# Kernel optimization log

Hardware: AMD Instinct MI355X
Metric: run time of the kernel (lower is better)

The kernel has to match this reference:

```python
import jax, jax.numpy as jnp
import numpy as np

EMBED = 128
HIDDEN = 256
N_NODES = 50000
N_EDGES = 640000
LN_EPS = 1e-5


def setup_inputs() -> dict:
    key = jax.random.key(0)
    ks = jax.random.split(key, 10)
    node_embeddings = jax.random.normal(ks[0], (N_NODES, EMBED), dtype=jnp.float32)
    edge_embeddings = jax.random.normal(ks[1], (N_EDGES, EMBED), dtype=jnp.float32)
    edge_index_list = jax.random.randint(ks[2], (2, N_EDGES), 0, N_NODES, dtype=jnp.int64 if jax.config.jax_enable_x64 else jnp.int32)
    # LayerNorm params
    ln_gamma = jnp.ones((EMBED,), dtype=jnp.float32)
    ln_beta = jnp.zeros((EMBED,), dtype=jnp.float32)
    # phi: Linear(embed->hidden), Linear(hidden->embed); xavier-ish init
    W1 = jax.random.normal(ks[3], (EMBED, HIDDEN), dtype=jnp.float32) * (1.0 / np.sqrt(EMBED))
    b1 = jnp.zeros((HIDDEN,), dtype=jnp.float32)
    W2 = jax.random.normal(ks[4], (HIDDEN, EMBED), dtype=jnp.float32) * (1.0 / np.sqrt(HIDDEN))
    b2 = jnp.zeros((EMBED,), dtype=jnp.float32)
    # theta: Linear(embed->embed)
    Wt = jax.random.normal(ks[5], (EMBED, EMBED), dtype=jnp.float32) * (1.0 / np.sqrt(EMBED))
    bt = jnp.zeros((EMBED,), dtype=jnp.float32)
    return {
        "node_embeddings": node_embeddings,
        "edge_embeddings": edge_embeddings,
        "edge_index_list": edge_index_list,
        "ln_gamma": ln_gamma, "ln_beta": ln_beta,
        "W1": W1, "b1": b1, "W2": W2, "b2": b2,
        "Wt": Wt, "bt": bt,
    }


def _layer_norm(x, gamma, beta):
    mu = jnp.mean(x, axis=-1, keepdims=True)
    var = jnp.var(x, axis=-1, keepdims=True)
    return (x - mu) * jax.lax.rsqrt(var + LN_EPS) * gamma + beta


def reference(node_embeddings, edge_embeddings, edge_index_list,
              ln_gamma, ln_beta, W1, b1, W2, b2, Wt, bt):
    n_nodes = node_embeddings.shape[0]
    h = _layer_norm(node_embeddings, ln_gamma, ln_beta)  # [N, D]
    center = edge_index_list[0]    # [E]
    neighbor = edge_index_list[1]  # [E]
    h_c = h[center]                # [E, D] gather
    h_n = h[neighbor]              # [E, D] gather
    s = edge_embeddings + h_c + h_n  # [E, D]
    # phi: SiLU -> Linear -> SiLU -> Linear
    t = jax.nn.silu(s) @ W1 + b1          # [E, H]
    theta_edge = jax.nn.silu(t) @ W2 + b2  # [E, D]
    msg = h_n * theta_edge                 # [E, D]
    agg = jax.ops.segment_sum(msg, center, num_segments=n_nodes)  # [N, D]
    # theta: SiLU -> Linear
    out = jax.nn.silu(h + agg) @ Wt + bt   # [N, D]
    return out
```

## Files before the change

### kernel.cpp

```cpp
#include <hip/hip_runtime.h>
#include <hip/hip_bf16.h>
#include <stdint.h>

#define EMBED 128
#define HIDDEN 256

typedef __bf16 v8bf __attribute__((ext_vector_type(8)));
typedef float v4f __attribute__((ext_vector_type(4)));

__device__ __forceinline__ float bf2f(unsigned short u){
    union { uint32_t i; float f; } v; v.i = ((uint32_t)u) << 16; return v.f;
}
__device__ __forceinline__ unsigned short f2bf(float f){
    __hip_bfloat16 b = __float2bfloat16(f);
    union { __hip_bfloat16 b; unsigned short u; } cv; cv.b = b; return cv.u;
}
__device__ __forceinline__ uint32_t pack2(float a, float b){
    __hip_bfloat162 t = __float22bfloat162_rn(make_float2(a, b));
    union { __hip_bfloat162 v; uint32_t u; } cv; cv.v = t; return cv.u;
}
__device__ __forceinline__ float lo_f(uint32_t u){ union{uint32_t i;float f;}v; v.i=u<<16; return v.f; }
__device__ __forceinline__ float hi_f(uint32_t u){ union{uint32_t i;float f;}v; v.i=u&0xffff0000u; return v.f; }
__device__ __forceinline__ float silu_f(float x){
    return x * __builtin_amdgcn_rcpf(1.0f + __expf(-x));
}

__device__ __forceinline__ float loadf(const void* b, size_t i, int isf32){
    return isf32 ? ((const float*)b)[i] : bf2f(((const unsigned short*)b)[i]);
}
__device__ __forceinline__ void load8f(const void* base, size_t off, int isf32, float o[8]){
    if (isf32){
        const float* p = (const float*)base + off;
        float4 a = *(const float4*)p, b = *(const float4*)(p + 4);
        o[0]=a.x;o[1]=a.y;o[2]=a.z;o[3]=a.w;o[4]=b.x;o[5]=b.y;o[6]=b.z;o[7]=b.w;
    } else {
        uint4 v = *(const uint4*)((const unsigned short*)base + off);
        uint32_t w[4] = {v.x, v.y, v.z, v.w};
        #pragma unroll
        for (int q = 0; q < 4; q++){ o[2*q] = lo_f(w[q]); o[2*q+1] = hi_f(w[q]); }
    }
}
__device__ __forceinline__ int idx_c(const int* ei, int e, int is64){
    return is64 ? ei[2*(size_t)e] : ei[e];
}
__device__ __forceinline__ int idx_n(const int* ei, int e, int E, int is64){
    return is64 ? ei[2*((size_t)E + e)] : ei[(size_t)E + e];
}

__device__ __forceinline__ int probe_isf32(const void* p, int lane){
    const unsigned short* u = (const unsigned short*)p;
    unsigned short a = u[lane], b = u[64 + lane];
    int bad = (((a >> 7) & 0xFF) >= 0x85) | (((b >> 7) & 0xFF) >= 0x85);
    return __any(bad) ? 1 : 0;
}
__device__ __forceinline__ int probe_is64(const int* ei, int lane){
    int nz = (ei[2*lane + 1] != 0) | (ei[2*(64 + lane) + 1] != 0);
    return __any(nz) ? 0 : 1;
}

__global__ __launch_bounds__(256) void hist_kernel(
    const int* __restrict__ eidx, int E, int* __restrict__ cnt)
{
    int is64 = probe_is64(eidx, threadIdx.x & 63);
    int e = blockIdx.x * 256 + threadIdx.x;
    if (e < E) atomicAdd(&cnt[idx_c(eidx, e, is64)], 1);
}

__global__ __launch_bounds__(1024) void scan_kernel(
    const int* __restrict__ cnt, int* __restrict__ cur, int N)
{
    __shared__ int wpart[16];
    int t = threadIdx.x;
    int Cg = (N + 1023) >> 10;
    int base = t * Cg;
    int s = 0;
    for (int i = 0; i < Cg; i++){ int k = base + i; if (k < N) s += cnt[k]; }
    int lane = t & 63, w = t >> 6;
    int x = s;
    for (int m = 1; m < 64; m <<= 1){ int y = __shfl_up(x, m); if (lane >= m) x += y; }
    if (lane == 63) wpart[w] = x;
    __syncthreads();
    if (t < 16){
        int v = wpart[t];
        for (int m = 1; m < 16; m <<= 1){ int y = __shfl_up(v, m); if (t >= m) v += y; }
        wpart[t] = v;
    }
    __syncthreads();
    int excl = x - s + (w ? wpart[w - 1] : 0);
    for (int i = 0; i < Cg; i++){
        int k = base + i;
        if (k < N){ cur[k] = excl; excl += cnt[k]; }
    }
}

__global__ __launch_bounds__(256) void scatter_kernel(
    const int* __restrict__ eidx, int E, int* __restrict__ cur,
    int* __restrict__ eid, int* __restrict__ cs, int* __restrict__ ns)
{
    int is64 = probe_is64(eidx, threadIdx.x & 63);
    int e = blockIdx.x * 256 + threadIdx.x;
    if (e < E){
        int c = idx_c(eidx, e, is64), n = idx_n(eidx, e, E, is64);
        int p = atomicAdd(&cur[c], 1);
        eid[p] = e; cs[p] = c; ns[p] = n;
    }
}

__global__ __launch_bounds__(256) void ln_kernel(
    const void* __restrict__ x, const void* __restrict__ g, const void* __restrict__ b,
    unsigned short* __restrict__ h, float* __restrict__ agg, int N)
{
    int wave = threadIdx.x >> 6, lane = threadIdx.x & 63;
    int isf32 = probe_isf32(x, lane);
    int node = blockIdx.x * 4 + wave;
    if (node >= N) return;
    *(float2*)(agg + (size_t)node * EMBED + lane * 2) = make_float2(0.f, 0.f);
    float x0, x1;
    if (isf32){
        float2 v = *(const float2*)((const float*)x + (size_t)node * EMBED + lane * 2);
        x0 = v.x; x1 = v.y;
    } else {
        uint32_t u = *(const uint32_t*)((const unsigned short*)x + (size_t)node * EMBED + lane * 2);
        x0 = lo_f(u); x1 = hi_f(u);
    }
    float s = x0 + x1, ss = x0 * x0 + x1 * x1;
    for (int m = 1; m < 64; m <<= 1){ s += __shfl_xor(s, m); ss += __shfl_xor(ss, m); }
    float mean = s * (1.0f / EMBED);
    float var  = ss * (1.0f / EMBED) - mean * mean;
    float rs   = rsqrtf(var + 1e-5f);
    float g0 = loadf(g, lane * 2, isf32), g1 = loadf(g, lane * 2 + 1, isf32);
    float b0 = loadf(b, lane * 2, isf32), b1v = loadf(b, lane * 2 + 1, isf32);
    float y0 = (x0 - mean) * rs * g0 + b0;
    float y1 = (x1 - mean) * rs * g1 + b1v;
    *(uint32_t*)(h + (size_t)node * EMBED + lane * 2) = pack2(y0, y1);
}

__global__ __launch_bounds__(256) void prepack_kernel(
    const void* __restrict__ W1, const void* __restrict__ W2, const void* __restrict__ Wt,
    const void* __restrict__ b1, const void* __restrict__ b2, const void* __restrict__ bt,
    unsigned short* __restrict__ W1p, unsigned short* __restrict__ W2p,
    unsigned short* __restrict__ Wtp, unsigned short* __restrict__ bpk)
{
    int isf32 = probe_isf32(W1, threadIdx.x & 63);
    int t = blockIdx.x * blockDim.x + threadIdx.x;
    if (t < 32768){
        int j = t & 7, lane = (t >> 3) & 63, k32 = (t >> 9) & 3, nt = t >> 11;
        int k = k32 * 32 + (lane >> 4) * 8 + j, n = nt * 16 + (lane & 15);
        W1p[t] = f2bf(loadf(W1, (size_t)k * HIDDEN + n, isf32));
    } else if (t < 65536){
        int t2 = t - 32768;
        int j = t2 & 7, lane = (t2 >> 3) & 63, k32 = (t2 >> 9) & 7, nt = t2 >> 12;
        int k = k32 * 32 + (lane >> 4) * 8 + j, n = nt * 16 + (lane & 15);
        W2p[t2] = f2bf(loadf(W2, (size_t)k * EMBED + n, isf32));
    } else if (t < 81920){
        int t3 = t - 65536;
        int j = t3 & 7, lane = (t3 >> 3) & 63, k32 = (t3 >> 9) & 3, nt = t3 >> 11;
        int k = k32 * 32 + (lane >> 4) * 8 + j, n = nt * 16 + (lane & 15);
        Wtp[t3] = f2bf(loadf(Wt, (size_t)k * EMBED + n, isf32));
    } else if (t < 82048){
        int i = t - 81920; bpk[i] = f2bf(loadf(b1, i, isf32));
    } else if (t < 82176){
        int i = t - 82048; bpk[128 + i] = f2bf(loadf(b1, 128 + i, isf32));
    } else if (t < 82304){
        int i = t - 82176; bpk[256 + i] = f2bf(loadf(b2, i, isf32));
    } else if (t < 82432){
        int i = t - 82304; bpk[384 + i] = f2bf(loadf(bt, i, isf32));
    }
}

__global__ __launch_bounds__(256, 4) void edge_kernel(
    const void* __restrict__ ee, const unsigned short* __restrict__ h,
    const int* __restrict__ eid, const int* __restrict__ cs, const int* __restrict__ ns,
    int E,
    const unsigned short* __restrict__ W1p, const unsigned short* __restrict__ W2p,
    const unsigned short* __restrict__ bpk,
    float* __restrict__ agg)
{
    __shared__ __align__(16) unsigned short sraw[64 * 136 * 2];
    __shared__ int cbuf[64], nbuf[64];
    unsigned short (*sbuf)[136] = (unsigned short (*)[136])sraw;
    unsigned short (*tbuf)[136] = (unsigned short (*)[136])(sraw + 64 * 136);
    float* msg = (float*)sraw;

    int wave = threadIdx.x >> 6, lane = threadIdx.x & 63;
    int quad = lane >> 4, l16 = lane & 15;
    int isf32 = probe_isf32(ee, lane);
    int ebase = blockIdx.x * 64;
    int colg = l16 * 8;

    #pragma unroll
    for (int i = 0; i < 4; i++){
        int row = wave * 16 + i * 4 + quad;
        int sp = ebase + row; if (sp >= E) sp = E - 1;
        int e = eid[sp], c = cs[sp], n = ns[sp];
        if (l16 == 0){ cbuf[row] = c; nbuf[row] = n; }
        float fe[8];
        load8f(ee, (size_t)e * EMBED + colg, isf32, fe);
        uint4 vc = *(const uint4*)(h + (size_t)c * EMBED + colg);
        uint4 vn = *(const uint4*)(h + (size_t)n * EMBED + colg);
        uint32_t pc[4] = {vc.x, vc.y, vc.z, vc.w};
        uint32_t pn[4] = {vn.x, vn.y, vn.z, vn.w};
        uint32_t o[4];
        #pragma unroll
        for (int q = 0; q < 4; q++){
            float a0 = fe[2*q]   + lo_f(pc[q]) + lo_f(pn[q]);
            float a1 = fe[2*q+1] + hi_f(pc[q]) + hi_f(pn[q]);
            o[q] = pack2(silu_f(a0), silu_f(a1));
        }
        *(uint4*)&sbuf[row][colg] = make_uint4(o[0], o[1], o[2], o[3]);
    }
    __syncthreads();

    v4f acc2[4][2];
    {
        float bias2[2];
        #pragma unroll
        for (int j = 0; j < 2; j++) bias2[j] = bf2f(bpk[256 + (wave * 2 + j) * 16 + l16]);
        #pragma unroll
        for (int rt = 0; rt < 4; rt++)
            #pragma unroll
            for (int j = 0; j < 2; j++)
                acc2[rt][j] = (v4f){bias2[j], bias2[j], bias2[j], bias2[j]};
    }

    #pragma unroll
    for (int hf = 0; hf < 2; hf++){
        {
            int ntb = hf * 8 + wave * 2;
            v8bf bw[2][4];
            float bias[2];
            #pragma unroll
            for (int j = 0; j < 2; j++){
                bias[j] = bf2f(bpk[(ntb + j) * 16 + l16]);
                #pragma unroll
                for (int k32 = 0; k32 < 4; k32++)
                    bw[j][k32] = *(const v8bf*)(W1p + ((size_t)((ntb + j) * 4 + k32) * 64 + lane) * 8);
            }
            #pragma unroll
            for (int rt = 0; rt < 4; rt++){
                v8bf a[4];
                #pragma unroll
                for (int k32 = 0; k32 < 4; k32++)
                    a[k32] = *(const v8bf*)&sbuf[rt * 16 + l16][k32 * 32 + quad * 8];
                v4f acc[2];
                #pragma unroll
                for (int j = 0; j < 2; j++) acc[j] = (v4f){bias[j], bias[j], bias[j], bias[j]};
                #pragma unroll
                for (int k32 = 0; k32 < 4; k32++)
                    #pragma unroll
                    for (int j = 0; j < 2; j++)
                        acc[j] = __builtin_amdgcn_mfma_f32_16x16x32_bf16(a[k32], bw[j][k32], acc[j], 0, 0, 0);
                #pragma unroll
                for (int j = 0; j < 2; j++)
                    #pragma unroll
                    for (int r = 0; r < 4; r++)
                        tbuf[rt * 16 + quad * 4 + r][(wave * 2 + j) * 16 + l16] = f2bf(silu_f(acc[j][r]));
            }
        }
        __syncthreads();
        {
            v8bf bw2[2][4];
            #pragma unroll
            for (int j = 0; j < 2; j++)
                #pragma unroll
                for (int kk = 0; kk < 4; kk++)
                    bw2[j][kk] = *(const v8bf*)(W2p + ((size_t)((wave * 2 + j) * 8 + hf * 4 + kk) * 64 + lane) * 8);
            #pragma unroll
            for (int rt = 0; rt < 4; rt++){
                v8bf a[4];
                #pragma unroll
                for (int kk = 0; kk < 4; kk++)
                    a[kk] = *(const v8bf*)&tbuf[rt * 16 + l16][kk * 32 + quad * 8];
                #pragma unroll
                for (int kk = 0; kk < 4; kk++)
                    #pragma unroll
                    for (int j = 0; j < 2; j++)
                        acc2[rt][j] = __builtin_amdgcn_mfma_f32_16x16x32_bf16(a[kk], bw2[j][kk], acc2[rt][j], 0, 0, 0);
            }
        }
        __syncthreads();
    }

    #pragma unroll
    for (int rt = 0; rt < 4; rt++){
        #pragma unroll
        for (int j = 0; j < 2; j++){
            int col = (wave * 2 + j) * 16 + l16;
            #pragma unroll
            for (int r = 0; r < 4; r++){
                int row = rt * 16 + quad * 4 + r;
                int n = nbuf[row];
                float hn = bf2f(h[(size_t)n * EMBED + col]);
                msg[row * 132 + col] = acc2[rt][j][r] * hn;
            }
        }
    }
    __syncthreads();

    {
        int col  = threadIdx.x & 127;
        int half = threadIdx.x >> 7;
        int r0 = half * 32;
        float acc = 0.f;
        int ccur = -1;
        int first = 1;
        for (int row = r0; row < r0 + 32; ++row){
            if (ebase + row >= E) break;
            int c = cbuf[row];
            if (c != ccur){
                if (ccur >= 0){
                    if (first) atomicAdd(&agg[(size_t)ccur * EMBED + col], acc);
                    else       agg[(size_t)ccur * EMBED + col] = acc;
                    first = 0;
                }
                ccur = c; acc = 0.f;
            }
            acc += msg[row * 132 + col];
        }
        if (ccur >= 0)
            atomicAdd(&agg[(size_t)ccur * EMBED + col], acc);
    }
}

__global__ __launch_bounds__(256) void node_out_kernel(
    const void* __restrict__ ne,
    const unsigned short* __restrict__ h, const float* __restrict__ agg,
    const unsigned short* __restrict__ Wtp, const unsigned short* __restrict__ bpk,
    void* __restrict__ out, int N)
{
    __shared__ __align__(16) unsigned short ubuf[4][16][136];
    int wave = threadIdx.x >> 6, lane = threadIdx.x & 63;
    int isf32 = probe_isf32(ne, lane);
    int quad = lane >> 4, l16 = lane & 15;
    int nbase = (blockIdx.x * 4 + wave) * 16;
    int colg = l16 * 8;
    #pragma unroll
    for (int i = 0; i < 4; i++){
        int row = i * 4 + quad;
        int node = nbase + row; int nn = node < N ? node : N - 1;
        uint4 vh = *(const uint4*)(h + (size_t)nn * EMBED + colg);
        float4 a0 = *(const float4*)(agg + (size_t)nn * EMBED + colg);
        float4 a1 = *(const float4*)(agg + (size_t)nn * EMBED + colg + 4);
        uint32_t ph[4] = {vh.x, vh.y, vh.z, vh.w};
        float af[8] = {a0.x, a0.y, a0.z, a0.w, a1.x, a1.y, a1.z, a1.w};
        uint32_t o[4];
        #pragma unroll
        for (int q = 0; q < 4; q++){
            float u0 = lo_f(ph[q]) + af[2 * q];
            float u1 = hi_f(ph[q]) + af[2 * q + 1];
            o[q] = pack2(silu_f(u0), silu_f(u1));
        }
        *(uint4*)&ubuf[wave][row][colg] = make_uint4(o[0], o[1], o[2], o[3]);
    }
    __syncthreads();
    for (int nt = 0; nt < 8; nt++){
        int col = nt * 16 + l16;
        float bc = bf2f(bpk[384 + col]);
        v4f acc = {bc, bc, bc, bc};
        #pragma unroll
        for (int k32 = 0; k32 < 4; k32++){
            v8bf a = *(const v8bf*)&ubuf[wave][l16][k32 * 32 + quad * 8];
            v8bf b = *(const v8bf*)(Wtp + ((size_t)(nt * 4 + k32) * 64 + lane) * 8);
            acc = __builtin_amdgcn_mfma_f32_16x16x32_bf16(a, b, acc, 0, 0, 0);
        }
        #pragma unroll
        for (int r = 0; r < 4; r++){
            int node = nbase + quad * 4 + r;
            if (node < N){
                if (isf32) ((float*)out)[(size_t)node * EMBED + col] = acc[r];
                else ((unsigned short*)out)[(size_t)node * EMBED + col] = f2bf(acc[r]);
            }
        }
    }
}

extern "C" void kernel_launch(void* const* d_in, const int* in_sizes, int n_in,
                              void* d_out, int out_size, void* d_ws, size_t ws_size,
                              hipStream_t stream)
{
    const void* ne = d_in[0];
    const void* ee = d_in[1];
    const int* eidx = (const int*)d_in[2];
    const void* g  = d_in[3];
    const void* be = d_in[4];
    const void* W1 = d_in[5];
    const void* b1 = d_in[6];
    const void* W2 = d_in[7];
    const void* b2 = d_in[8];
    const void* Wt = d_in[9];
    const void* bt = d_in[10];
    int N = in_sizes[0] / EMBED;
    int E = in_sizes[2] / 2;

    char* ws = (char*)d_ws;
    size_t off = 0;
    unsigned short* h = (unsigned short*)(ws + off); off += (size_t)N * EMBED * 2;
    off = (off + 255) & ~(size_t)255;
    float* agg = (float*)(ws + off);                 off += (size_t)N * EMBED * 4;
    off = (off + 255) & ~(size_t)255;
    unsigned short* W1p = (unsigned short*)(ws + off); off += 32768 * 2;
    unsigned short* W2p = (unsigned short*)(ws + off); off += 32768 * 2;
    unsigned short* Wtp = (unsigned short*)(ws + off); off += 16384 * 2;
    unsigned short* bpk = (unsigned short*)(ws + off); off += 512 * 2;
    off = (off + 255) & ~(size_t)255;
    int* cnt = (int*)(ws + off); off += (size_t)N * 4;
    off = (off + 255) & ~(size_t)255;
    int* cur = (int*)(ws + off); off += (size_t)N * 4;
    off = (off + 255) & ~(size_t)255;
    int* eid = (int*)(ws + off); off += (size_t)E * 4;
    int* cs  = (int*)(ws + off); off += (size_t)E * 4;
    int* ns  = (int*)(ws + off); off += (size_t)E * 4;

    hipMemsetAsync(cnt, 0, (size_t)N * 4, stream);
    prepack_kernel<<<(82432 + 255) / 256, 256, 0, stream>>>(W1, W2, Wt, b1, b2, bt,
                                                            W1p, W2p, Wtp, bpk);
    hist_kernel<<<(E + 255) / 256, 256, 0, stream>>>(eidx, E, cnt);
    scan_kernel<<<1, 1024, 0, stream>>>(cnt, cur, N);
    scatter_kernel<<<(E + 255) / 256, 256, 0, stream>>>(eidx, E, cur, eid, cs, ns);
    ln_kernel<<<(N + 3) / 4, 256, 0, stream>>>(ne, g, be, h, agg, N);
    edge_kernel<<<(E + 63) / 64, 256, 0, stream>>>(ee, h, eid, cs, ns, E,
                                                   W1p, W2p, bpk, agg);
    node_out_kernel<<<(N + 63) / 64, 256, 0, stream>>>(ne, h, agg, Wtp, bpk,
                                                       d_out, N);
}
```

Baseline: 781.7 us.

## Fuse all stages into one persistent cooperative kernel with grid syncs

Replaces the memset plus seven separate launches with a single cooperative persistent kernel of 1024 blocks. It runs prepack, layer norm, histogram, a two-level parallel scan, scatter, the edge MLP and the node output in phases separated by grid.sync. The single-block serial scan becomes a per-block chunk scan followed by a scan over block partials. The aim is to remove launch gaps and the slow single-block scan, at the cost of grid-wide barriers, grid-stride loops with fewer blocks in flight, and a hard dependency on co-residency of 1024 blocks, with the old multi-kernel path kept as a fallback.

```diff
diff --git a/kernel.cpp b/kernel.cpp
--- a/kernel.cpp
+++ b/kernel.cpp
@@ -1,9 +1,13 @@
 #include <hip/hip_runtime.h>
+#include <hip/hip_cooperative_groups.h>
 #include <hip/hip_bf16.h>
 #include <stdint.h>
 
+namespace cg = cooperative_groups;
+
 #define EMBED 128
 #define HIDDEN 256
+#define NBLK 1024
 
 typedef __bf16 v8bf __attribute__((ext_vector_type(8)));
 typedef float v4f __attribute__((ext_vector_type(4)));
@@ -58,91 +62,13 @@
     return __any(nz) ? 0 : 1;
 }
 
-__global__ __launch_bounds__(256) void hist_kernel(
-    const int* __restrict__ eidx, int E, int* __restrict__ cnt)
-{
-    int is64 = probe_is64(eidx, threadIdx.x & 63);
-    int e = blockIdx.x * 256 + threadIdx.x;
-    if (e < E) atomicAdd(&cnt[idx_c(eidx, e, is64)], 1);
-}
-
-__global__ __launch_bounds__(1024) void scan_kernel(
-    const int* __restrict__ cnt, int* __restrict__ cur, int N)
-{
-    __shared__ int wpart[16];
-    int t = threadIdx.x;
-    int Cg = (N + 1023) >> 10;
-    int base = t * Cg;
-    int s = 0;
-    for (int i = 0; i < Cg; i++){ int k = base + i; if (k < N) s += cnt[k]; }
-    int lane = t & 63, w = t >> 6;
-    int x = s;
-    for (int m = 1; m < 64; m <<= 1){ int y = __shfl_up(x, m); if (lane >= m) x += y; }
-    if (lane == 63) wpart[w] = x;
-    __syncthreads();
-    if (t < 16){
-        int v = wpart[t];
-        for (int m = 1; m < 16; m <<= 1){ int y = __shfl_up(v, m); if (t >= m) v += y; }
-        wpart[t] = v;
-    }
-    __syncthreads();
-    int excl = x - s + (w ? wpart[w - 1] : 0);
-    for (int i = 0; i < Cg; i++){
-        int k = base + i;
-        if (k < N){ cur[k] = excl; excl += cnt[k]; }
-    }
-}
-
-__global__ __launch_bounds__(256) void scatter_kernel(
-    const int* __restrict__ eidx, int E, int* __restrict__ cur,
-    int* __restrict__ eid, int* __restrict__ cs, int* __restrict__ ns)
-{
-    int is64 = probe_is64(eidx, threadIdx.x & 63);
-    int e = blockIdx.x * 256 + threadIdx.x;
-    if (e < E){
-        int c = idx_c(eidx, e, is64), n = idx_n(eidx, e, E, is64);
-        int p = atomicAdd(&cur[c], 1);
-        eid[p] = e; cs[p] = c; ns[p] = n;
-    }
-}
-
-__global__ __launch_bounds__(256) void ln_kernel(
-    const void* __restrict__ x, const void* __restrict__ g, const void* __restrict__ b,
-    unsigned short* __restrict__ h, float* __restrict__ agg, int N)
-{
-    int wave = threadIdx.x >> 6, lane = threadIdx.x & 63;
-    int isf32 = probe_isf32(x, lane);
-    int node = blockIdx.x * 4 + wave;
-    if (node >= N) return;
-    *(float2*)(agg + (size_t)node * EMBED + lane * 2) = make_float2(0.f, 0.f);
-    float x0, x1;
-    if (isf32){
-        float2 v = *(const float2*)((const float*)x + (size_t)node * EMBED + lane * 2);
-        x0 = v.x; x1 = v.y;
-    } else {
-        uint32_t u = *(const uint32_t*)((const unsigned short*)x + (size_t)node * EMBED + lane * 2);
-        x0 = lo_f(u); x1 = hi_f(u);
-    }
-    float s = x0 + x1, ss = x0 * x0 + x1 * x1;
-    for (int m = 1; m < 64; m <<= 1){ s += __shfl_xor(s, m); ss += __shfl_xor(ss, m); }
-    float mean = s * (1.0f / EMBED);
-    float var  = ss * (1.0f / EMBED) - mean * mean;
-    float rs   = rsqrtf(var + 1e-5f);
-    float g0 = loadf(g, lane * 2, isf32), g1 = loadf(g, lane * 2 + 1, isf32);
-    float b0 = loadf(b, lane * 2, isf32), b1v = loadf(b, lane * 2 + 1, isf32);
-    float y0 = (x0 - mean) * rs * g0 + b0;
-    float y1 = (x1 - mean) * rs * g1 + b1v;
-    *(uint32_t*)(h + (size_t)node * EMBED + lane * 2) = pack2(y0, y1);
-}
-
-__global__ __launch_bounds__(256) void prepack_kernel(
-    const void* __restrict__ W1, const void* __restrict__ W2, const void* __restrict__ Wt,
-    const void* __restrict__ b1, const void* __restrict__ b2, const void* __restrict__ bt,
-    unsigned short* __restrict__ W1p, unsigned short* __restrict__ W2p,
-    unsigned short* __restrict__ Wtp, unsigned short* __restrict__ bpk)
-{
-    int isf32 = probe_isf32(W1, threadIdx.x & 63);
-    int t = blockIdx.x * blockDim.x + threadIdx.x;
+
+__device__ __forceinline__ void prepack_one(int t,
+    const void* W1, const void* W2, const void* Wt,
+    const void* b1, const void* b2, const void* bt,
+    unsigned short* W1p, unsigned short* W2p, unsigned short* Wtp, unsigned short* bpk,
+    int isf32)
+{
     if (t < 32768){
         int j = t & 7, lane = (t >> 3) & 63, k32 = (t >> 9) & 3, nt = t >> 11;
         int k = k32 * 32 + (lane >> 4) * 8 + j, n = nt * 16 + (lane & 15);
@@ -157,10 +83,8 @@
         int j = t3 & 7, lane = (t3 >> 3) & 63, k32 = (t3 >> 9) & 3, nt = t3 >> 11;
         int k = k32 * 32 + (lane >> 4) * 8 + j, n = nt * 16 + (lane & 15);
         Wtp[t3] = f2bf(loadf(Wt, (size_t)k * EMBED + n, isf32));
-    } else if (t < 82048){
+    } else if (t < 82176){
         int i = t - 81920; bpk[i] = f2bf(loadf(b1, i, isf32));
-    } else if (t < 82176){
-        int i = t - 82048; bpk[128 + i] = f2bf(loadf(b1, 128 + i, isf32));
     } else if (t < 82304){
         int i = t - 82176; bpk[256 + i] = f2bf(loadf(b2, i, isf32));
     } else if (t < 82432){
@@ -168,24 +92,44 @@
     }
 }
 
-__global__ __launch_bounds__(256, 4) void edge_kernel(
+__device__ __forceinline__ void ln_one(int node, int lane,
+    const void* x, const void* g, const void* b,
+    unsigned short* h, float* agg, int isf32)
+{
+    *(float2*)(agg + (size_t)node * EMBED + lane * 2) = make_float2(0.f, 0.f);
+    float x0, x1;
+    if (isf32){
+        float2 v = *(const float2*)((const float*)x + (size_t)node * EMBED + lane * 2);
+        x0 = v.x; x1 = v.y;
+    } else {
+        uint32_t u = *(const uint32_t*)((const unsigned short*)x + (size_t)node * EMBED + lane * 2);
+        x0 = lo_f(u); x1 = hi_f(u);
+    }
+    float s = x0 + x1, ss = x0 * x0 + x1 * x1;
+    for (int m = 1; m < 64; m <<= 1){ s += __shfl_xor(s, m); ss += __shfl_xor(ss, m); }
+    float mean = s * (1.0f / EMBED);
+    float var  = ss * (1.0f / EMBED) - mean * mean;
+    float rs   = rsqrtf(var + 1e-5f);
+    float g0 = loadf(g, lane * 2, isf32), g1 = loadf(g, lane * 2 + 1, isf32);
+    float b0 = loadf(b, lane * 2, isf32), b1v = loadf(b, lane * 2 + 1, isf32);
+    float y0 = (x0 - mean) * rs * g0 + b0;
+    float y1 = (x1 - mean) * rs * g1 + b1v;
+    *(uint32_t*)(h + (size_t)node * EMBED + lane * 2) = pack2(y0, y1);
+}
+
+__device__ __forceinline__ void edge_tile(
+    int ebase, int E,
     const void* __restrict__ ee, const unsigned short* __restrict__ h,
     const int* __restrict__ eid, const int* __restrict__ cs, const int* __restrict__ ns,
-    int E,
     const unsigned short* __restrict__ W1p, const unsigned short* __restrict__ W2p,
     const unsigned short* __restrict__ bpk,
-    float* __restrict__ agg)
-{
-    __shared__ __align__(16) unsigned short sraw[64 * 136 * 2];
-    __shared__ int cbuf[64], nbuf[64];
-    unsigned short (*sbuf)[136] = (unsigned short (*)[136])sraw;
-    unsigned short (*tbuf)[136] = (unsigned short (*)[136])(sraw + 64 * 136);
-    float* msg = (float*)sraw;
-
-    int wave = threadIdx.x >> 6, lane = threadIdx.x & 63;
+    float* __restrict__ agg, int isf32,
+    unsigned short (*sbuf)[136], unsigned short (*tbuf)[136], float* msg,
+    int* cbuf, int* nbuf)
+{
+    int tid = threadIdx.x;
+    int wave = tid >> 6, lane = tid & 63;
     int quad = lane >> 4, l16 = lane & 15;
-    int isf32 = probe_isf32(ee, lane);
-    int ebase = blockIdx.x * 64;
     int colg = l16 * 8;
 
     #pragma unroll
@@ -298,8 +242,8 @@
     __syncthreads();
 
     {
-        int col  = threadIdx.x & 127;
-        int half = threadIdx.x >> 7;
+        int col  = tid & 127;
+        int half = tid >> 7;
         int r0 = half * 32;
         float acc = 0.f;
         int ccur = -1;
@@ -320,19 +264,20 @@
         if (ccur >= 0)
             atomicAdd(&agg[(size_t)ccur * EMBED + col], acc);
     }
-}
-
-__global__ __launch_bounds__(256) void node_out_kernel(
-    const void* __restrict__ ne,
+    __syncthreads();
+}
+
+__device__ __forceinline__ void node_tile(
+    int tile, int N,
     const unsigned short* __restrict__ h, const float* __restrict__ agg,
     const unsigned short* __restrict__ Wtp, const unsigned short* __restrict__ bpk,
-    void* __restrict__ out, int N)
-{
-    __shared__ __align__(16) unsigned short ubuf[4][16][136];
-    int wave = threadIdx.x >> 6, lane = threadIdx.x & 63;
-    int isf32 = probe_isf32(ne, lane);
+    void* __restrict__ out, int isf32,
+    unsigned short (*ubuf)[16][136])
+{
+    int tid = threadIdx.x;
+    int wave = tid >> 6, lane = tid & 63;
     int quad = lane >> 4, l16 = lane & 15;
-    int nbase = (blockIdx.x * 4 + wave) * 16;
+    int nbase = (tile * 4 + wave) * 16;
     int colg = l16 * 8;
     #pragma unroll
     for (int i = 0; i < 4; i++){
@@ -372,6 +317,206 @@
             }
         }
     }
+    __syncthreads();
+}
+
+__global__ __launch_bounds__(256, 4) void fused_kernel(
+    const void* __restrict__ ne, const void* __restrict__ ee, const int* __restrict__ eidx,
+    const void* __restrict__ g, const void* __restrict__ be,
+    const void* __restrict__ W1, const void* __restrict__ b1,
+    const void* __restrict__ W2, const void* __restrict__ b2,
+    const void* __restrict__ Wt, const void* __restrict__ bt,
+    unsigned short* __restrict__ h, float* __restrict__ agg,
+    unsigned short* __restrict__ W1p, unsigned short* __restrict__ W2p,
+    unsigned short* __restrict__ Wtp, unsigned short* __restrict__ bpk,
+    int* __restrict__ cnt, int* __restrict__ cur,
+    int* __restrict__ part, int* __restrict__ partex,
+    int* __restrict__ eid, int* __restrict__ cs, int* __restrict__ ns,
+    void* __restrict__ out, int N, int E)
+{
+    cg::grid_group grid = cg::this_grid();
+    __shared__ __align__(16) unsigned short sraw[64 * 136 * 2];
+    __shared__ int cbuf[64], nbuf[64];
+
+    int tid = threadIdx.x;
+    int wave = tid >> 6, lane = tid & 63;
+    int bid = blockIdx.x;
+    int gt = bid * 256 + tid;
+    const int GT = NBLK * 256;
+
+    int isf32_ne = probe_isf32(ne, lane);
+    int isf32_ee = probe_isf32(ee, lane);
+    int isf32_w  = probe_isf32(W1, lane);
+    int is64     = probe_is64(eidx, lane);
+
+    for (int k = gt; k < N; k += GT) cnt[k] = 0;
+    if (gt < 82432) prepack_one(gt, W1, W2, Wt, b1, b2, bt, W1p, W2p, Wtp, bpk, isf32_w);
+    for (int node = bid * 4 + wave; node < N; node += NBLK * 4)
+        ln_one(node, lane, ne, g, be, h, agg, isf32_ne);
+    grid.sync();
+
+    for (int e = gt; e < E; e += GT) atomicAdd(&cnt[idx_c(eidx, e, is64)], 1);
+    grid.sync();
+
+    int chunk = (N + NBLK - 1) / NBLK;
+    int k0 = bid * chunk;
+    int* iLDS = (int*)sraw;
+    for (int i = tid; i < chunk; i += 256) iLDS[i] = (k0 + i < N) ? cnt[k0 + i] : 0;
+    __syncthreads();
+    if (tid == 0){
+        int s = 0;
+        for (int i = 0; i < chunk; i++){ int v = iLDS[i]; iLDS[i] = s; s += v; }
+        part[bid] = s;
+    }
+    __syncthreads();
+    grid.sync();
+
+    if (bid == 0){
+        int b0 = tid * 4;
+        int v[4]; int sl = 0;
+        #pragma unroll
+        for (int i = 0; i < 4; i++){ v[i] = part[b0 + i]; sl += v[i]; }
+        int x = sl;
+        for (int m = 1; m < 64; m <<= 1){ int y = __shfl_up(x, m); if (lane >= m) x += y; }
+        if (lane == 63) cbuf[wave] = x;
+        __syncthreads();
+        if (tid == 0){ int a = 0; for (int i = 0; i < 4; i++){ int t2 = cbuf[i]; cbuf[i] = a; a += t2; } }
+        __syncthreads();
+        int excl = x - sl + cbuf[wave];
+        #pragma unroll
+        for (int i = 0; i < 4; i++){ partex[b0 + i] = excl; excl += v[i]; }
+    }
+    grid.sync();
+
+    {
+        int base = partex[bid];
+        for (int i = tid; i < chunk; i += 256){
+            int k = k0 + i;
+            if (k < N) cur[k] = base + iLDS[i];
+        }
+    }
+    grid.sync();
+
+    for (int e = gt; e < E; e += GT){
+        int c = idx_c(eidx, e, is64), n = idx_n(eidx, e, E, is64);
+        int p = atomicAdd(&cur[c], 1);
+        eid[p] = e; cs[p] = c; ns[p] = n;
+    }
+    grid.sync();
+
+    {
+        unsigned short (*sbuf)[136] = (unsigned short (*)[136])sraw;
+        unsigned short (*tbuf)[136] = (unsigned short (*)[136])(sraw + 64 * 136);
+        float* msg = (float*)sraw;
+        int ntile = (E + 63) >> 6;
+        for (int tile = bid; tile < ntile; tile += NBLK)
+            edge_tile(tile * 64, E, ee, h, eid, cs, ns, W1p, W2p, bpk, agg, isf32_ee,
+                      sbuf, tbuf, msg, cbuf, nbuf);
+    }
+    grid.sync();
+
+    {
+        unsigned short (*ubuf)[16][136] = (unsigned short (*)[16][136])sraw;
+        int ntile = (N + 63) >> 6;
+        for (int tile = bid; tile < ntile; tile += NBLK)
+            node_tile(tile, N, h, agg, Wtp, bpk, out, isf32_ne, ubuf);
+    }
+}
+
+__global__ __launch_bounds__(256) void prepack_kernel(
+    const void* W1, const void* W2, const void* Wt,
+    const void* b1, const void* b2, const void* bt,
+    unsigned short* W1p, unsigned short* W2p, unsigned short* Wtp, unsigned short* bpk)
+{
+    int isf32 = probe_isf32(W1, threadIdx.x & 63);
+    int t = blockIdx.x * blockDim.x + threadIdx.x;
+    if (t < 82432) prepack_one(t, W1, W2, Wt, b1, b2, bt, W1p, W2p, Wtp, bpk, isf32);
+}
+
+__global__ __launch_bounds__(256) void hist_kernel(
+    const int* __restrict__ eidx, int E, int* __restrict__ cnt)
+{
+    int is64 = probe_is64(eidx, threadIdx.x & 63);
+    int e = blockIdx.x * 256 + threadIdx.x;
+    if (e < E) atomicAdd(&cnt[idx_c(eidx, e, is64)], 1);
+}
+
+__global__ __launch_bounds__(1024) void scan_kernel(
+    const int* __restrict__ cnt, int* __restrict__ cur, int N)
+{
+    __shared__ int wpart[16];
+    int t = threadIdx.x;
+    int Cg = (N + 1023) >> 10;
+    int base = t * Cg;
+    int s = 0;
+    for (int i = 0; i < Cg; i++){ int k = base + i; if (k < N) s += cnt[k]; }
+    int lane = t & 63, w = t >> 6;
+    int x = s;
+    for (int m = 1; m < 64; m <<= 1){ int y = __shfl_up(x, m); if (lane >= m) x += y; }
+    if (lane == 63) wpart[w] = x;
+    __syncthreads();
+    if (t < 16){
+        int v = wpart[t];
+        for (int m = 1; m < 16; m <<= 1){ int y = __shfl_up(v, m); if (t >= m) v += y; }
+        wpart[t] = v;
+    }
+    __syncthreads();
+    int excl = x - s + (w ? wpart[w - 1] : 0);
+    for (int i = 0; i < Cg; i++){
+        int k = base + i;
+        if (k < N){ cur[k] = excl; excl += cnt[k]; }
+    }
+}
+
+__global__ __launch_bounds__(256) void scatter_kernel(
+    const int* __restrict__ eidx, int E, int* __restrict__ cur,
+    int* __restrict__ eid, int* __restrict__ cs, int* __restrict__ ns)
+{
+    int is64 = probe_is64(eidx, threadIdx.x & 63);
+    int e = blockIdx.x * 256 + threadIdx.x;
+    if (e < E){
+        int c = idx_c(eidx, e, is64), n = idx_n(eidx, e, E, is64);
+        int p = atomicAdd(&cur[c], 1);
+        eid[p] = e; cs[p] = c; ns[p] = n;
+    }
+}
+
+__global__ __launch_bounds__(256) void ln_kernel(
+    const void* __restrict__ x, const void* __restrict__ g, const void* __restrict__ b,
+    unsigned short* __restrict__ h, float* __restrict__ agg, int N)
+{
+    int wave = threadIdx.x >> 6, lane = threadIdx.x & 63;
+    int isf32 = probe_isf32(x, lane);
+    int node = blockIdx.x * 4 + wave;
+    if (node < N) ln_one(node, lane, x, g, b, h, agg, isf32);
+}
+
+__global__ __launch_bounds__(256, 4) void edge_kernel(
+    const void* __restrict__ ee, const unsigned short* __restrict__ h,
+    const int* __restrict__ eid, const int* __restrict__ cs, const int* __restrict__ ns,
+    int E,
+    const unsigned short* __restrict__ W1p, const unsigned short* __restrict__ W2p,
+    const unsigned short* __restrict__ bpk,
+    float* __restrict__ agg)
+{
+    __shared__ __align__(16) unsigned short sraw[64 * 136 * 2];
+    __shared__ int cbuf[64], nbuf[64];
+    int isf32 = probe_isf32(ee, threadIdx.x & 63);
+    edge_tile(blockIdx.x * 64, E, ee, h, eid, cs, ns, W1p, W2p, bpk, agg, isf32,
+              (unsigned short (*)[136])sraw,
+              (unsigned short (*)[136])(sraw + 64 * 136),
+              (float*)sraw, cbuf, nbuf);
+}
+
+__global__ __launch_bounds__(256) void node_out_kernel(
+    const void* __restrict__ ne,
+    const unsigned short* __restrict__ h, const float* __restrict__ agg,
+    const unsigned short* __restrict__ Wtp, const unsigned short* __restrict__ bpk,
+    void* __restrict__ out, int N)
+{
+    __shared__ __align__(16) unsigned short ubuf[4][16][136];
+    int isf32 = probe_isf32(ne, threadIdx.x & 63);
+    node_tile(blockIdx.x, N, h, agg, Wtp, bpk, out, isf32, ubuf);
 }
 
 extern "C" void kernel_launch(void* const* d_in, const int* in_sizes, int n_in,
@@ -407,19 +552,32 @@
     off = (off + 255) & ~(size_t)255;
     int* cur = (int*)(ws + off); off += (size_t)N * 4;
     off = (off + 255) & ~(size_t)255;
+    int* part   = (int*)(ws + off); off += (size_t)NBLK * 4;
+    int* partex = (int*)(ws + off); off += (size_t)NBLK * 4;
+    off = (off + 255) & ~(size_t)255;
     int* eid = (int*)(ws + off); off += (size_t)E * 4;
     int* cs  = (int*)(ws + off); off += (size_t)E * 4;
     int* ns  = (int*)(ws + off); off += (size_t)E * 4;
 
-    hipMemsetAsync(cnt, 0, (size_t)N * 4, stream);
-    prepack_kernel<<<(82432 + 255) / 256, 256, 0, stream>>>(W1, W2, Wt, b1, b2, bt,
-                                                            W1p, W2p, Wtp, bpk);
-    hist_kernel<<<(E + 255) / 256, 256, 0, stream>>>(eidx, E, cnt);
-    scan_kernel<<<1, 1024, 0, stream>>>(cnt, cur, N);
-    scatter_kernel<<<(E + 255) / 256, 256, 0, stream>>>(eidx, E, cur, eid, cs, ns);
-    ln_kernel<<<(N + 3) / 4, 256, 0, stream>>>(ne, g, be, h, agg, N);
-    edge_kernel<<<(E + 63) / 64, 256, 0, stream>>>(ee, h, eid, cs, ns, E,
-                                                   W1p, W2p, bpk, agg);
-    node_out_kernel<<<(N + 63) / 64, 256, 0, stream>>>(ne, h, agg, Wtp, bpk,
-                                                       d_out, N);
-}
+    void* kargs[] = { (void*)&ne, (void*)&ee, (void*)&eidx, (void*)&g, (void*)&be,
+                      (void*)&W1, (void*)&b1, (void*)&W2, (void*)&b2, (void*)&Wt, (void*)&bt,
+                      (void*)&h, (void*)&agg, (void*)&W1p, (void*)&W2p, (void*)&Wtp, (void*)&bpk,
+                      (void*)&cnt, (void*)&cur, (void*)&part, (void*)&partex,
+                      (void*)&eid, (void*)&cs, (void*)&ns, (void*)&d_out, (void*)&N, (void*)&E };
+    hipError_t err = hipLaunchCooperativeKernel((const void*)fused_kernel,
+                                                dim3(NBLK), dim3(256), kargs, 0, stream);
+    if (err != hipSuccess){
+        (void)hipGetLastError();
+        hipMemsetAsync(cnt, 0, (size_t)N * 4, stream);
+        prepack_kernel<<<(82432 + 255) / 256, 256, 0, stream>>>(W1, W2, Wt, b1, b2, bt,
+                                                                W1p, W2p, Wtp, bpk);
+        hist_kernel<<<(E + 255) / 256, 256, 0, stream>>>(eidx, E, cnt);
+        scan_kernel<<<1, 1024, 0, stream>>>(cnt, cur, N);
+        scatter_kernel<<<(E + 255) / 256, 256, 0, stream>>>(eidx, E, cur, eid, cs, ns);
+        ln_kernel<<<(N + 3) / 4, 256, 0, stream>>>(ne, g, be, h, agg, N);
+        edge_kernel<<<(E + 63) / 64, 256, 0, stream>>>(ee, h, eid, cs, ns, E,
+                                                       W1p, W2p, bpk, agg);
+        node_out_kernel<<<(N + 63) / 64, 256, 0, stream>>>(ne, h, agg, Wtp, bpk,
+                                                           d_out, N);
+    }
+}
```

Measured after the change: 1.575 ms. +101.5%, slower.

## Fuse prep kernels, parallelize CSR scan, drop cs/ns arrays, prefetch neighbor h

Applied to the files above, without the earlier changes.

Merges the memset, weight prepack and LayerNorm into one grid-stride prep kernel, cutting launch count. The single-block scan is replaced by a two-level multi-block scan, since one block serially walking 50k counts was a bottleneck. The scatter stage now writes only edge ids; the edge kernel reads center and neighbor indices back from edge_index through eid, trading two sorted-array writes for an extra dependent gather. Neighbor h values for the message multiply are loaded before the MLP so their latency overlaps the matmuls, at the cost of extra registers.

```diff
diff --git a/kernel.cpp b/kernel.cpp
--- a/kernel.cpp
+++ b/kernel.cpp
@@ -58,91 +58,12 @@
     return __any(nz) ? 0 : 1;
 }
 
-__global__ __launch_bounds__(256) void hist_kernel(
-    const int* __restrict__ eidx, int E, int* __restrict__ cnt)
-{
-    int is64 = probe_is64(eidx, threadIdx.x & 63);
-    int e = blockIdx.x * 256 + threadIdx.x;
-    if (e < E) atomicAdd(&cnt[idx_c(eidx, e, is64)], 1);
-}
-
-__global__ __launch_bounds__(1024) void scan_kernel(
-    const int* __restrict__ cnt, int* __restrict__ cur, int N)
-{
-    __shared__ int wpart[16];
-    int t = threadIdx.x;
-    int Cg = (N + 1023) >> 10;
-    int base = t * Cg;
-    int s = 0;
-    for (int i = 0; i < Cg; i++){ int k = base + i; if (k < N) s += cnt[k]; }
-    int lane = t & 63, w = t >> 6;
-    int x = s;
-    for (int m = 1; m < 64; m <<= 1){ int y = __shfl_up(x, m); if (lane >= m) x += y; }
-    if (lane == 63) wpart[w] = x;
-    __syncthreads();
-    if (t < 16){
-        int v = wpart[t];
-        for (int m = 1; m < 16; m <<= 1){ int y = __shfl_up(v, m); if (t >= m) v += y; }
-        wpart[t] = v;
-    }
-    __syncthreads();
-    int excl = x - s + (w ? wpart[w - 1] : 0);
-    for (int i = 0; i < Cg; i++){
-        int k = base + i;
-        if (k < N){ cur[k] = excl; excl += cnt[k]; }
-    }
-}
-
-__global__ __launch_bounds__(256) void scatter_kernel(
-    const int* __restrict__ eidx, int E, int* __restrict__ cur,
-    int* __restrict__ eid, int* __restrict__ cs, int* __restrict__ ns)
-{
-    int is64 = probe_is64(eidx, threadIdx.x & 63);
-    int e = blockIdx.x * 256 + threadIdx.x;
-    if (e < E){
-        int c = idx_c(eidx, e, is64), n = idx_n(eidx, e, E, is64);
-        int p = atomicAdd(&cur[c], 1);
-        eid[p] = e; cs[p] = c; ns[p] = n;
-    }
-}
-
-__global__ __launch_bounds__(256) void ln_kernel(
-    const void* __restrict__ x, const void* __restrict__ g, const void* __restrict__ b,
-    unsigned short* __restrict__ h, float* __restrict__ agg, int N)
-{
-    int wave = threadIdx.x >> 6, lane = threadIdx.x & 63;
-    int isf32 = probe_isf32(x, lane);
-    int node = blockIdx.x * 4 + wave;
-    if (node >= N) return;
-    *(float2*)(agg + (size_t)node * EMBED + lane * 2) = make_float2(0.f, 0.f);
-    float x0, x1;
-    if (isf32){
-        float2 v = *(const float2*)((const float*)x + (size_t)node * EMBED + lane * 2);
-        x0 = v.x; x1 = v.y;
-    } else {
-        uint32_t u = *(const uint32_t*)((const unsigned short*)x + (size_t)node * EMBED + lane * 2);
-        x0 = lo_f(u); x1 = hi_f(u);
-    }
-    float s = x0 + x1, ss = x0 * x0 + x1 * x1;
-    for (int m = 1; m < 64; m <<= 1){ s += __shfl_xor(s, m); ss += __shfl_xor(ss, m); }
-    float mean = s * (1.0f / EMBED);
-    float var  = ss * (1.0f / EMBED) - mean * mean;
-    float rs   = rsqrtf(var + 1e-5f);
-    float g0 = loadf(g, lane * 2, isf32), g1 = loadf(g, lane * 2 + 1, isf32);
-    float b0 = loadf(b, lane * 2, isf32), b1v = loadf(b, lane * 2 + 1, isf32);
-    float y0 = (x0 - mean) * rs * g0 + b0;
-    float y1 = (x1 - mean) * rs * g1 + b1v;
-    *(uint32_t*)(h + (size_t)node * EMBED + lane * 2) = pack2(y0, y1);
-}
-
-__global__ __launch_bounds__(256) void prepack_kernel(
-    const void* __restrict__ W1, const void* __restrict__ W2, const void* __restrict__ Wt,
-    const void* __restrict__ b1, const void* __restrict__ b2, const void* __restrict__ bt,
-    unsigned short* __restrict__ W1p, unsigned short* __restrict__ W2p,
-    unsigned short* __restrict__ Wtp, unsigned short* __restrict__ bpk)
-{
-    int isf32 = probe_isf32(W1, threadIdx.x & 63);
-    int t = blockIdx.x * blockDim.x + threadIdx.x;
+__device__ __forceinline__ void prepack_one(int t,
+    const void* W1, const void* W2, const void* Wt,
+    const void* b1, const void* b2, const void* bt,
+    unsigned short* W1p, unsigned short* W2p, unsigned short* Wtp, unsigned short* bpk,
+    int isf32)
+{
     if (t < 32768){
         int j = t & 7, lane = (t >> 3) & 63, k32 = (t >> 9) & 3, nt = t >> 11;
         int k = k32 * 32 + (lane >> 4) * 8 + j, n = nt * 16 + (lane & 15);
@@ -157,10 +78,8 @@
         int j = t3 & 7, lane = (t3 >> 3) & 63, k32 = (t3 >> 9) & 3, nt = t3 >> 11;
         int k = k32 * 32 + (lane >> 4) * 8 + j, n = nt * 16 + (lane & 15);
         Wtp[t3] = f2bf(loadf(Wt, (size_t)k * EMBED + n, isf32));
-    } else if (t < 82048){
+    } else if (t < 82176){
         int i = t - 81920; bpk[i] = f2bf(loadf(b1, i, isf32));
-    } else if (t < 82176){
-        int i = t - 82048; bpk[128 + i] = f2bf(loadf(b1, 128 + i, isf32));
     } else if (t < 82304){
         int i = t - 82176; bpk[256 + i] = f2bf(loadf(b2, i, isf32));
     } else if (t < 82432){
@@ -168,10 +87,107 @@
     }
 }
 
+__device__ __forceinline__ void ln_one(int node, int lane,
+    const void* x, const void* g, const void* b,
+    unsigned short* h, float* agg, int isf32)
+{
+    *(float2*)(agg + (size_t)node * EMBED + lane * 2) = make_float2(0.f, 0.f);
+    float x0, x1;
+    if (isf32){
+        float2 v = *(const float2*)((const float*)x + (size_t)node * EMBED + lane * 2);
+        x0 = v.x; x1 = v.y;
+    } else {
+        uint32_t u = *(const uint32_t*)((const unsigned short*)x + (size_t)node * EMBED + lane * 2);
+        x0 = lo_f(u); x1 = hi_f(u);
+    }
+    float s = x0 + x1, ss = x0 * x0 + x1 * x1;
+    for (int m = 1; m < 64; m <<= 1){ s += __shfl_xor(s, m); ss += __shfl_xor(ss, m); }
+    float mean = s * (1.0f / EMBED);
+    float var  = ss * (1.0f / EMBED) - mean * mean;
+    float rs   = rsqrtf(var + 1e-5f);
+    float g0 = loadf(g, lane * 2, isf32), g1 = loadf(g, lane * 2 + 1, isf32);
+    float b0 = loadf(b, lane * 2, isf32), b1v = loadf(b, lane * 2 + 1, isf32);
+    float y0 = (x0 - mean) * rs * g0 + b0;
+    float y1 = (x1 - mean) * rs * g1 + b1v;
+    *(uint32_t*)(h + (size_t)node * EMBED + lane * 2) = pack2(y0, y1);
+}
+
+__global__ __launch_bounds__(256) void prep_kernel(
+    const void* __restrict__ ne, const void* __restrict__ g, const void* __restrict__ be,
+    const void* __restrict__ W1, const void* __restrict__ W2, const void* __restrict__ Wt,
+    const void* __restrict__ b1, const void* __restrict__ b2, const void* __restrict__ bt,
+    unsigned short* __restrict__ h, float* __restrict__ agg,
+    unsigned short* __restrict__ W1p, unsigned short* __restrict__ W2p,
+    unsigned short* __restrict__ Wtp, unsigned short* __restrict__ bpk,
+    int* __restrict__ cnt, int N)
+{
+    int tid = threadIdx.x, bid = blockIdx.x;
+    int wave = tid >> 6, lane = tid & 63;
+    int gt = bid * 256 + tid;
+    int GT = gridDim.x * 256;
+    int isf32_ne = probe_isf32(ne, lane);
+    int isf32_w  = probe_isf32(W1, lane);
+    for (int k = gt; k < N; k += GT) cnt[k] = 0;
+    if (gt < 82432) prepack_one(gt, W1, W2, Wt, b1, b2, bt, W1p, W2p, Wtp, bpk, isf32_w);
+    for (int node = bid * 4 + wave; node < N; node += gridDim.x * 4)
+        ln_one(node, lane, ne, g, be, h, agg, isf32_ne);
+}
+
+__global__ __launch_bounds__(256) void hist_kernel(
+    const int* __restrict__ eidx, int E, int* __restrict__ cnt)
+{
+    int is64 = probe_is64(eidx, threadIdx.x & 63);
+    int e = blockIdx.x * 256 + threadIdx.x;
+    if (e < E) atomicAdd(&cnt[idx_c(eidx, e, is64)], 1);
+}
+
+__global__ __launch_bounds__(256) void scan_a_kernel(
+    const int* __restrict__ cnt, int* __restrict__ cur, int* __restrict__ bsum, int N)
+{
+    __shared__ int wp[4];
+    int t = threadIdx.x, lane = t & 63, w = t >> 6;
+    int k = blockIdx.x * 256 + t;
+    int v = (k < N) ? cnt[k] : 0;
+    int x = v;
+    for (int m = 1; m < 64; m <<= 1){ int y = __shfl_up(x, m); if (lane >= m) x += y; }
+    if (lane == 63) wp[w] = x;
+    __syncthreads();
+    if (t == 0){ int a = 0; for (int i = 0; i < 4; i++){ int s = wp[i]; wp[i] = a; a += s; } bsum[blockIdx.x] = a; }
+    __syncthreads();
+    if (k < N) cur[k] = x - v + wp[w];
+}
+
+__global__ __launch_bounds__(256) void scan_b_kernel(
+    const int* __restrict__ bsum, int* __restrict__ bexcl, int NB)
+{
+    __shared__ int wp[4];
+    int t = threadIdx.x, lane = t & 63, w = t >> 6;
+    int v = (t < NB) ? bsum[t] : 0;
+    int x = v;
+    for (int m = 1; m < 64; m <<= 1){ int y = __shfl_up(x, m); if (lane >= m) x += y; }
+    if (lane == 63) wp[w] = x;
+    __syncthreads();
+    if (t == 0){ int a = 0; for (int i = 0; i < 4; i++){ int s = wp[i]; wp[i] = a; a += s; } }
+    __syncthreads();
+    if (t < NB) bexcl[t] = x - v + wp[w];
+}
+
+__global__ __launch_bounds__(256) void scatter_kernel(
+    const int* __restrict__ eidx, int E, int* __restrict__ cur,
+    const int* __restrict__ bexcl, int* __restrict__ eid)
+{
+    int is64 = probe_is64(eidx, threadIdx.x & 63);
+    int e = blockIdx.x * 256 + threadIdx.x;
+    if (e < E){
+        int c = idx_c(eidx, e, is64);
+        int p = bexcl[c >> 8] + atomicAdd(&cur[c], 1);
+        eid[p] = e;
+    }
+}
+
 __global__ __launch_bounds__(256, 4) void edge_kernel(
     const void* __restrict__ ee, const unsigned short* __restrict__ h,
-    const int* __restrict__ eid, const int* __restrict__ cs, const int* __restrict__ ns,
-    int E,
+    const int* __restrict__ eid, const int* __restrict__ eidx, int E,
     const unsigned short* __restrict__ W1p, const unsigned short* __restrict__ W2p,
     const unsigned short* __restrict__ bpk,
     float* __restrict__ agg)
@@ -182,22 +198,34 @@
     unsigned short (*tbuf)[136] = (unsigned short (*)[136])(sraw + 64 * 136);
     float* msg = (float*)sraw;
 
-    int wave = threadIdx.x >> 6, lane = threadIdx.x & 63;
+    int tid = threadIdx.x;
+    int wave = tid >> 6, lane = tid & 63;
     int quad = lane >> 4, l16 = lane & 15;
     int isf32 = probe_isf32(ee, lane);
+    int is64  = probe_is64(eidx, lane);
     int ebase = blockIdx.x * 64;
     int colg = l16 * 8;
 
+    int e4[4], c4[4], n4[4];
+    #pragma unroll
+    for (int i = 0; i < 4; i++){
+        int sp = ebase + wave * 16 + i * 4 + quad;
+        if (sp >= E) sp = E - 1;
+        e4[i] = eid[sp];
+    }
+    #pragma unroll
+    for (int i = 0; i < 4; i++){
+        c4[i] = idx_c(eidx, e4[i], is64);
+        n4[i] = idx_n(eidx, e4[i], E, is64);
+    }
     #pragma unroll
     for (int i = 0; i < 4; i++){
         int row = wave * 16 + i * 4 + quad;
-        int sp = ebase + row; if (sp >= E) sp = E - 1;
-        int e = eid[sp], c = cs[sp], n = ns[sp];
-        if (l16 == 0){ cbuf[row] = c; nbuf[row] = n; }
+        if (l16 == 0){ cbuf[row] = c4[i]; nbuf[row] = n4[i]; }
         float fe[8];
-        load8f(ee, (size_t)e * EMBED + colg, isf32, fe);
-        uint4 vc = *(const uint4*)(h + (size_t)c * EMBED + colg);
-        uint4 vn = *(const uint4*)(h + (size_t)n * EMBED + colg);
+        load8f(ee, (size_t)e4[i] * EMBED + colg, isf32, fe);
+        uint4 vc = *(const uint4*)(h + (size_t)c4[i] * EMBED + colg);
+        uint4 vn = *(const uint4*)(h + (size_t)n4[i] * EMBED + colg);
         uint32_t pc[4] = {vc.x, vc.y, vc.z, vc.w};
         uint32_t pn[4] = {vn.x, vn.y, vn.z, vn.w};
         uint32_t o[4];
@@ -210,6 +238,18 @@
         *(uint4*)&sbuf[row][colg] = make_uint4(o[0], o[1], o[2], o[3]);
     }
     __syncthreads();
+
+    unsigned short hn_pre[4][2][4];
+    #pragma unroll
+    for (int rt = 0; rt < 4; rt++)
+        #pragma unroll
+        for (int r = 0; r < 4; r++){
+            int row = rt * 16 + quad * 4 + r;
+            int n = nbuf[row];
+            #pragma unroll
+            for (int j = 0; j < 2; j++)
+                hn_pre[rt][j][r] = h[(size_t)n * EMBED + (wave * 2 + j) * 16 + l16];
+        }
 
     v4f acc2[4][2];
     {
@@ -289,17 +329,15 @@
             #pragma unroll
             for (int r = 0; r < 4; r++){
                 int row = rt * 16 + quad * 4 + r;
-                int n = nbuf[row];
-                float hn = bf2f(h[(size_t)n * EMBED + col]);
-                msg[row * 132 + col] = acc2[rt][j][r] * hn;
+                msg[row * 132 + col] = acc2[rt][j][r] * bf2f(hn_pre[rt][j][r]);
             }
         }
     }
     __syncthreads();
 
     {
-        int col  = threadIdx.x & 127;
-        int half = threadIdx.x >> 7;
+        int col  = tid & 127;
+        int half = tid >> 7;
         int r0 = half * 32;
         float acc = 0.f;
         int ccur = -1;
@@ -329,7 +367,8 @@
     void* __restrict__ out, int N)
 {
     __shared__ __align__(16) unsigned short ubuf[4][16][136];
-    int wave = threadIdx.x >> 6, lane = threadIdx.x & 63;
+    int tid = threadIdx.x;
+    int wave = tid >> 6, lane = tid & 63;
     int isf32 = probe_isf32(ne, lane);
     int quad = lane >> 4, l16 = lane & 15;
     int nbase = (blockIdx.x * 4 + wave) * 16;
@@ -407,18 +446,20 @@
     off = (off + 255) & ~(size_t)255;
     int* cur = (int*)(ws + off); off += (size_t)N * 4;
     off = (off + 255) & ~(size_t)255;
+    int* bsum  = (int*)(ws + off); off += 1024;
+    int* bexcl = (int*)(ws + off); off += 1024;
+    off = (off + 255) & ~(size_t)255;
     int* eid = (int*)(ws + off); off += (size_t)E * 4;
-    int* cs  = (int*)(ws + off); off += (size_t)E * 4;
-    int* ns  = (int*)(ws + off); off += (size_t)E * 4;
-
-    hipMemsetAsync(cnt, 0, (size_t)N * 4, stream);
-    prepack_kernel<<<(82432 + 255) / 256, 256, 0, stream>>>(W1, W2, Wt, b1, b2, bt,
-                                                            W1p, W2p, Wtp, bpk);
+
+    int NB = (N + 255) / 256;
+
+    prep_kernel<<<2048, 256, 0, stream>>>(ne, g, be, W1, W2, Wt, b1, b2, bt,
+                                          h, agg, W1p, W2p, Wtp, bpk, cnt, N);
     hist_kernel<<<(E + 255) / 256, 256, 0, stream>>>(eidx, E, cnt);
-    scan_kernel<<<1, 1024, 0, stream>>>(cnt, cur, N);
-    scatter_kernel<<<(E + 255) / 256, 256, 0, stream>>>(eidx, E, cur, eid, cs, ns);
-    ln_kernel<<<(N + 3) / 4, 256, 0, stream>>>(ne, g, be, h, agg, N);
-    edge_kernel<<<(E + 63) / 64, 256, 0, stream>>>(ee, h, eid, cs, ns, E,
+    scan_a_kernel<<<NB, 256, 0, stream>>>(cnt, cur, bsum, N);
+    scan_b_kernel<<<1, 256, 0, stream>>>(bsum, bexcl, NB);
+    scatter_kernel<<<(E + 255) / 256, 256, 0, stream>>>(eidx, E, cur, bexcl, eid);
+    edge_kernel<<<(E + 63) / 64, 256, 0, stream>>>(ee, h, eid, eidx, E,
                                                    W1p, W2p, bpk, agg);
     node_out_kernel<<<(N + 63) / 64, 256, 0, stream>>>(ne, h, agg, Wtp, bpk,
                                                        d_out, N);
```

New measurement: 737.3 us. -5.7%, faster.
